# Kernel tuning notes

Measured on AMD Instinct MI355X. Metric: run time of the kernel, lower is better.

## Reference

```python
import jax, jax.numpy as jnp
import numpy as np

S = 2        # downscale
REDUCE = 32  # QK channel dim


def _to_grid(x):
    # [B,C,H,W] -> [B,C,H/S,W/S,S*S], matching ConverToGrid (reshape+permute+reshape)
    B, C, H, W = x.shape
    h, w = H // S, W // S
    x = x.reshape(B, C, h, S, w, S)
    x = x.transpose(0, 1, 2, 4, 3, 5)
    return x.reshape(B, C, h, w, S * S)


def setup_inputs() -> dict:
    key = jax.random.key(0)
    k1, k2, k3 = jax.random.split(key, 3)
    fm = jax.random.normal(k1, (8, 128, 256, 256), dtype=jnp.float32)
    Wq = jax.random.normal(k2, (REDUCE, 128), dtype=jnp.float32) * 0.05
    Wk = jax.random.normal(k3, (REDUCE, 128), dtype=jnp.float32) * 0.05
    return {"fm": fm, "Wq": Wq, "Wk": Wk}


def reference(fm, Wq, Wk):
    B, C, H, W = fm.shape
    h, w = H // S, W // S
    # Q branch: AvgPool2d(S,S) -> 1x1 conv -> scale by 1/sqrt(reduce)
    pooled = fm.reshape(B, C, h, S, w, S).mean(axis=(3, 5))          # [B,C,h,w]
    Q = jnp.einsum('rc,bchw->brhw', Wq, pooled) / jnp.sqrt(
        jnp.asarray(REDUCE, fm.dtype))                               # [B,r,h,w]
    # K branch: 1x1 conv -> grid
    K = _to_grid(jnp.einsum('rc,bchw->brhw', Wk, fm))                # [B,r,h,w,S*S]
    # V branch: grid of raw features
    V = _to_grid(fm)                                                 # [B,C,h,w,S*S]
    # sum over channel dim of Q*K, softmax over window dim (dropout p=0 => identity)
    logits = jnp.einsum('brhw,brhws->bhws', Q, K)                    # [B,h,w,S*S]
    attn = jax.nn.softmax(logits, axis=-1)
    # weighted sum over window positions
    out = jnp.einsum('bchws,bhws->bchw', V, attn)                    # [B,C,h,w]
    return out
```

## Files before the change

### kernel.cpp

```cpp
#include <hip/hip_runtime.h>
#include <hip/hip_bf16.h>
#include <math.h>


typedef unsigned int uint32;

__device__ __forceinline__ uint32 pack2(float x, float y) {
  union { __hip_bfloat162 h; uint32 u; } cvt;
  cvt.h = __float22bfloat162_rn(make_float2(x, y));
  return cvt.u;
}
__device__ __forceinline__ float2 unpack2(uint32 u) {
  float2 r;
  r.x = __uint_as_float(u << 16);
  r.y = __uint_as_float(u & 0xffff0000u);
  return r;
}

__global__ __launch_bounds__(256) void wt_kernel(const float* __restrict__ Wq,
                                                 const float* __restrict__ Wk,
                                                 float* __restrict__ ws) {
  int t = blockIdx.x * 256 + threadIdx.x;
  if (t < 4096) {
    int c = t >> 5, r = t & 31;
    ws[c * 32 + r]        = Wq[r * 128 + c] * (0.25f / sqrtf(32.0f));
    ws[4096 + c * 32 + r] = Wk[r * 128 + c];
  }
}

__global__ __launch_bounds__(512)
void attn_main(const float* __restrict__ fm,
               const float* __restrict__ ws,
               float* __restrict__ out) {
  __shared__ float Qpart[4 * 32 * 64];
  __shared__ float lbuf[8 * 64 * 4];
  __shared__ float abuf[64 * 4];

  const int tid = threadIdx.x;
  const int p   = tid & 63;
  const int g   = __builtin_amdgcn_readfirstlane(tid >> 6);

  const int blk = blockIdx.x;
  const int w0  = (blk & 1) * 64;
  const int h   = (blk >> 1) & 127;
  const int b   = blk >> 8;
  const int cb  = g * 16;

  const float* gbase = fm + ((size_t)(b * 128 + cb) * 65536) +
                       (size_t)(2 * h) * 256 + 2 * (w0 + p);
  const float* wq = ws + cb * 32;
  const float* wk = ws + 4096 + cb * 32;

  uint32 pka[16], pkb[16];
  {
    const float* gp = gbase;
#pragma unroll
    for (int i = 0; i < 16; ++i) {
      const float2 va = *(const float2*)(gp);
      const float2 vb = *(const float2*)(gp + 256);
      pka[i] = pack2(va.x, va.y);
      pkb[i] = pack2(vb.x, vb.y);
      gp += 65536;
    }
  }

  float qa[32];
#pragma unroll
  for (int r = 0; r < 32; ++r) qa[r] = 0.f;
#pragma unroll
  for (int i = 0; i < 16; ++i) {
    const float2 va = unpack2(pka[i]);
    const float2 vb = unpack2(pkb[i]);
    const float u = (va.x + va.y) + (vb.x + vb.y);
#pragma unroll
    for (int r = 0; r < 32; ++r)
      qa[r] = fmaf(wq[i * 32 + r], u, qa[r]);
  }

  if (g >= 4) {
#pragma unroll
    for (int r = 0; r < 32; ++r) Qpart[(g - 4) * 2048 + r * 64 + p] = qa[r];
  }
  __syncthreads();
  if (g < 4) {
#pragma unroll
    for (int r = 0; r < 32; ++r) Qpart[g * 2048 + r * 64 + p] += qa[r];
  }
  __syncthreads();
  if (g < 2) {
#pragma unroll
    for (int r = 0; r < 32; ++r)
      Qpart[g * 2048 + r * 64 + p] += Qpart[(g + 2) * 2048 + r * 64 + p];
  }
  __syncthreads();
#pragma unroll
  for (int r = 0; r < 32; ++r)
    qa[r] = Qpart[r * 64 + p] + Qpart[2048 + r * 64 + p];

  float l0 = 0.f, l1 = 0.f, l2 = 0.f, l3 = 0.f;
#pragma unroll
  for (int i = 0; i < 16; ++i) {
    const float2 va = unpack2(pka[i]);
    const float2 vb = unpack2(pkb[i]);
    float t0 = 0.f, t1 = 0.f;
#pragma unroll
    for (int r = 0; r < 32; r += 2) {
      t0 = fmaf(qa[r + 0], wk[i * 32 + r + 0], t0);
      t1 = fmaf(qa[r + 1], wk[i * 32 + r + 1], t1);
    }
    const float tv = t0 + t1;
    l0 = fmaf(tv, va.x, l0);
    l1 = fmaf(tv, va.y, l1);
    l2 = fmaf(tv, vb.x, l2);
    l3 = fmaf(tv, vb.y, l3);
  }
  *(float4*)(lbuf + (g * 64 + p) * 4) = make_float4(l0, l1, l2, l3);
  __syncthreads();

  if (tid < 64) {
    float L0 = 0.f, L1 = 0.f, L2 = 0.f, L3 = 0.f;
#pragma unroll
    for (int k = 0; k < 8; ++k) {
      const float4 s = *(const float4*)(lbuf + (k * 64 + tid) * 4);
      L0 += s.x; L1 += s.y; L2 += s.z; L3 += s.w;
    }
    const float mx = fmaxf(fmaxf(L0, L1), fmaxf(L2, L3));
    const float e0 = __expf(L0 - mx), e1 = __expf(L1 - mx);
    const float e2 = __expf(L2 - mx), e3 = __expf(L3 - mx);
    const float inv = 1.0f / ((e0 + e1) + (e2 + e3));
    *(float4*)(abuf + tid * 4) =
        make_float4(e0 * inv, e1 * inv, e2 * inv, e3 * inv);
  }
  __syncthreads();
  const float4 at = *(const float4*)(abuf + p * 4);

  {
    float* op = out + ((size_t)(b * 128 + cb) * 16384) + h * 128 + w0 + p;
#pragma unroll
    for (int i = 0; i < 16; ++i) {
      const float2 va = unpack2(pka[i]);
      const float2 vb = unpack2(pkb[i]);
      op[(size_t)i * 16384] =
          fmaf(at.x, va.x, fmaf(at.y, va.y, fmaf(at.z, vb.x, at.w * vb.y)));
    }
  }
}

extern "C" void kernel_launch(void* const* d_in, const int* in_sizes, int n_in,
                              void* d_out, int out_size, void* d_ws, size_t ws_size,
                              hipStream_t stream) {
  const float* fm = (const float*)d_in[0];
  const float* Wq = (const float*)d_in[1];
  const float* Wk = (const float*)d_in[2];
  float* outp = (float*)d_out;
  float* ws = (float*)d_ws;

  wt_kernel<<<16, 256, 0, stream>>>(Wq, Wk, ws);
  attn_main<<<2048, 512, 0, stream>>>(fm, ws, outp);
}
```

Measured before the change: 138.3 us.

## Stage packed fm tile and bf16 weights in LDS with 256-thread blocks

```diff
diff --git a/kernel.cpp b/kernel.cpp
--- a/kernel.cpp
+++ b/kernel.cpp
@@ -4,6 +4,8 @@
 
 
 typedef unsigned int uint32;
+typedef const __attribute__((address_space(1))) void* gas_t;
+typedef __attribute__((address_space(3))) void* las_t;
 
 __device__ __forceinline__ uint32 pack2(float x, float y) {
   union { __hip_bfloat162 h; uint32 u; } cvt;
@@ -19,111 +21,152 @@
 
 __global__ __launch_bounds__(256) void wt_kernel(const float* __restrict__ Wq,
                                                  const float* __restrict__ Wk,
-                                                 float* __restrict__ ws) {
+                                                 uint32* __restrict__ ws) {
   int t = blockIdx.x * 256 + threadIdx.x;
-  if (t < 4096) {
-    int c = t >> 5, r = t & 31;
-    ws[c * 32 + r]        = Wq[r * 128 + c] * (0.25f / sqrtf(32.0f));
-    ws[4096 + c * 32 + r] = Wk[r * 128 + c];
-  }
-}
-
-__global__ __launch_bounds__(512)
+  if (t < 2048) {
+    int c = t >> 4, j = t & 15;
+    const float s = 0.25f / sqrtf(32.0f);
+    ws[c * 16 + j] = pack2(Wq[(2 * j) * 128 + c] * s,
+                           Wq[(2 * j + 1) * 128 + c] * s);
+    ws[2048 + c * 16 + j] = pack2(Wk[(2 * j) * 128 + c],
+                                  Wk[(2 * j + 1) * 128 + c]);
+  }
+}
+
+__global__ __launch_bounds__(256, 4)
 void attn_main(const float* __restrict__ fm,
-               const float* __restrict__ ws,
+               const uint32* __restrict__ ws,
                float* __restrict__ out) {
-  __shared__ float Qpart[4 * 32 * 64];
-  __shared__ float lbuf[8 * 64 * 4];
-  __shared__ float abuf[64 * 4];
+  extern __shared__ char smem[];
+  uint2*  stash = (uint2*)smem;
+  uint32* wbuf  = (uint32*)(smem + 65536);
+  float*  Qbuf  = (float*)(smem + 73728);
+  float*  lbuf  = Qbuf;
+  float*  abuf  = Qbuf + 1024;
 
   const int tid = threadIdx.x;
   const int p   = tid & 63;
-  const int g   = __builtin_amdgcn_readfirstlane(tid >> 6);
+  const int w   = __builtin_amdgcn_readfirstlane(tid >> 6);
+  const int cb  = 32 * w;
 
   const int blk = blockIdx.x;
   const int w0  = (blk & 1) * 64;
   const int h   = (blk >> 1) & 127;
   const int b   = blk >> 8;
-  const int cb  = g * 16;
-
-  const float* gbase = fm + ((size_t)(b * 128 + cb) * 65536) +
-                       (size_t)(2 * h) * 256 + 2 * (w0 + p);
-  const float* wq = ws + cb * 32;
-  const float* wk = ws + 4096 + cb * 32;
-
-  uint32 pka[16], pkb[16];
-  {
-    const float* gp = gbase;
+
 #pragma unroll
-    for (int i = 0; i < 16; ++i) {
-      const float2 va = *(const float2*)(gp);
-      const float2 vb = *(const float2*)(gp + 256);
-      pka[i] = pack2(va.x, va.y);
-      pkb[i] = pack2(vb.x, vb.y);
-      gp += 65536;
+  for (int j = 0; j < 8; ++j) Qbuf[tid * 8 + j] = 0.f;
+
+  {
+    const char* src = (const char*)ws + tid * 16;
+    char* dst = (char*)wbuf + tid * 16;
+    __builtin_amdgcn_global_load_lds((gas_t)src, (las_t)dst, 16, 0, 0);
+    __builtin_amdgcn_global_load_lds((gas_t)(src + 4096), (las_t)(dst + 4096),
+                                     16, 0, 0);
+  }
+
+  {
+    const float* g = fm + ((size_t)(b * 128 + cb)) * 65536 +
+                     (size_t)(2 * h) * 256 + 2 * (w0 + p);
+#pragma unroll 8
+    for (int c = 0; c < 32; ++c) {
+      const float2 va = *(const float2*)(g + (size_t)c * 65536);
+      const float2 vb = *(const float2*)(g + (size_t)c * 65536 + 256);
+      stash[(cb + c) * 64 + p] =
+          make_uint2(pack2(va.x, va.y), pack2(vb.x, vb.y));
     }
   }
-
-  float qa[32];
+  asm volatile("s_waitcnt vmcnt(0)" ::: "memory");
+  __syncthreads();
+
+#define QFMA(word, r0)                              \
+  {                                                 \
+    const float2 f = unpack2(word);                 \
+    Qacc[r0] = fmaf(f.x, u, Qacc[r0]);              \
+    Qacc[(r0) + 1] = fmaf(f.y, u, Qacc[(r0) + 1]);  \
+  }
+
+  float Qacc[32];
 #pragma unroll
-  for (int r = 0; r < 32; ++r) qa[r] = 0.f;
+  for (int r = 0; r < 32; ++r) Qacc[r] = 0.f;
+#pragma unroll 4
+  for (int c = 0; c < 32; ++c) {
+    const int cc = cb + c;
+    const uint2 sv = stash[cc * 64 + p];
+    const float2 va = unpack2(sv.x);
+    const float2 vb = unpack2(sv.y);
+    const float u = (va.x + va.y) + (vb.x + vb.y);
+    const uint4 wa = *(const uint4*)(wbuf + cc * 16);
+    const uint4 wb = *(const uint4*)(wbuf + cc * 16 + 4);
+    const uint4 wc = *(const uint4*)(wbuf + cc * 16 + 8);
+    const uint4 wd = *(const uint4*)(wbuf + cc * 16 + 12);
+    QFMA(wa.x, 0)  QFMA(wa.y, 2)  QFMA(wa.z, 4)  QFMA(wa.w, 6)
+    QFMA(wb.x, 8)  QFMA(wb.y, 10) QFMA(wb.z, 12) QFMA(wb.w, 14)
+    QFMA(wc.x, 16) QFMA(wc.y, 18) QFMA(wc.z, 20) QFMA(wc.w, 22)
+    QFMA(wd.x, 24) QFMA(wd.y, 26) QFMA(wd.z, 28) QFMA(wd.w, 30)
+  }
+#undef QFMA
+  __syncthreads();
+
+  {
+    const char* src = (const char*)ws + 8192 + tid * 16;
+    char* dst = (char*)wbuf + tid * 16;
+    __builtin_amdgcn_global_load_lds((gas_t)src, (las_t)dst, 16, 0, 0);
+    __builtin_amdgcn_global_load_lds((gas_t)(src + 4096), (las_t)(dst + 4096),
+                                     16, 0, 0);
+  }
+#pragma unroll 8
+  for (int r = 0; r < 32; ++r) atomicAdd(&Qbuf[r * 64 + p], Qacc[r]);
+  asm volatile("s_waitcnt vmcnt(0)" ::: "memory");
+  __syncthreads();
+
+  float qh[32];
 #pragma unroll
-  for (int i = 0; i < 16; ++i) {
-    const float2 va = unpack2(pka[i]);
-    const float2 vb = unpack2(pkb[i]);
-    const float u = (va.x + va.y) + (vb.x + vb.y);
-#pragma unroll
-    for (int r = 0; r < 32; ++r)
-      qa[r] = fmaf(wq[i * 32 + r], u, qa[r]);
-  }
-
-  if (g >= 4) {
-#pragma unroll
-    for (int r = 0; r < 32; ++r) Qpart[(g - 4) * 2048 + r * 64 + p] = qa[r];
-  }
-  __syncthreads();
-  if (g < 4) {
-#pragma unroll
-    for (int r = 0; r < 32; ++r) Qpart[g * 2048 + r * 64 + p] += qa[r];
-  }
-  __syncthreads();
-  if (g < 2) {
-#pragma unroll
-    for (int r = 0; r < 32; ++r)
-      Qpart[g * 2048 + r * 64 + p] += Qpart[(g + 2) * 2048 + r * 64 + p];
-  }
-  __syncthreads();
-#pragma unroll
-  for (int r = 0; r < 32; ++r)
-    qa[r] = Qpart[r * 64 + p] + Qpart[2048 + r * 64 + p];
+  for (int r = 0; r < 32; ++r) qh[r] = Qbuf[r * 64 + p];
+  __syncthreads();
+
+#define TFMA(word, r0)                      \
+  {                                         \
+    const float2 f = unpack2(word);         \
+    t0 = fmaf(qh[r0], f.x, t0);             \
+    t1 = fmaf(qh[(r0) + 1], f.y, t1);       \
+  }
 
   float l0 = 0.f, l1 = 0.f, l2 = 0.f, l3 = 0.f;
-#pragma unroll
-  for (int i = 0; i < 16; ++i) {
-    const float2 va = unpack2(pka[i]);
-    const float2 vb = unpack2(pkb[i]);
+#pragma unroll 4
+  for (int c = 0; c < 32; ++c) {
+    const int cc = cb + c;
+    const uint4 wa = *(const uint4*)(wbuf + cc * 16);
+    const uint4 wb = *(const uint4*)(wbuf + cc * 16 + 4);
+    const uint4 wc = *(const uint4*)(wbuf + cc * 16 + 8);
+    const uint4 wd = *(const uint4*)(wbuf + cc * 16 + 12);
     float t0 = 0.f, t1 = 0.f;
-#pragma unroll
-    for (int r = 0; r < 32; r += 2) {
-      t0 = fmaf(qa[r + 0], wk[i * 32 + r + 0], t0);
-      t1 = fmaf(qa[r + 1], wk[i * 32 + r + 1], t1);
-    }
+    TFMA(wa.x, 0)  TFMA(wa.y, 2)  TFMA(wa.z, 4)  TFMA(wa.w, 6)
+    TFMA(wb.x, 8)  TFMA(wb.y, 10) TFMA(wb.z, 12) TFMA(wb.w, 14)
+    TFMA(wc.x, 16) TFMA(wc.y, 18) TFMA(wc.z, 20) TFMA(wc.w, 22)
+    TFMA(wd.x, 24) TFMA(wd.y, 26) TFMA(wd.z, 28) TFMA(wd.w, 30)
     const float tv = t0 + t1;
+    const uint2 sv = stash[cc * 64 + p];
+    const float2 va = unpack2(sv.x);
+    const float2 vb = unpack2(sv.y);
     l0 = fmaf(tv, va.x, l0);
     l1 = fmaf(tv, va.y, l1);
     l2 = fmaf(tv, vb.x, l2);
     l3 = fmaf(tv, vb.y, l3);
   }
-  *(float4*)(lbuf + (g * 64 + p) * 4) = make_float4(l0, l1, l2, l3);
+#undef TFMA
+  *(float4*)(lbuf + (w * 64 + p) * 4) = make_float4(l0, l1, l2, l3);
   __syncthreads();
 
   if (tid < 64) {
-    float L0 = 0.f, L1 = 0.f, L2 = 0.f, L3 = 0.f;
-#pragma unroll
-    for (int k = 0; k < 8; ++k) {
-      const float4 s = *(const float4*)(lbuf + (k * 64 + tid) * 4);
-      L0 += s.x; L1 += s.y; L2 += s.z; L3 += s.w;
-    }
+    const float4 s0 = *(const float4*)(lbuf + (0 * 64 + tid) * 4);
+    const float4 s1 = *(const float4*)(lbuf + (1 * 64 + tid) * 4);
+    const float4 s2 = *(const float4*)(lbuf + (2 * 64 + tid) * 4);
+    const float4 s3 = *(const float4*)(lbuf + (3 * 64 + tid) * 4);
+    const float L0 = (s0.x + s1.x) + (s2.x + s3.x);
+    const float L1 = (s0.y + s1.y) + (s2.y + s3.y);
+    const float L2 = (s0.z + s1.z) + (s2.z + s3.z);
+    const float L3 = (s0.w + s1.w) + (s2.w + s3.w);
     const float mx = fmaxf(fmaxf(L0, L1), fmaxf(L2, L3));
     const float e0 = __expf(L0 - mx), e1 = __expf(L1 - mx);
     const float e2 = __expf(L2 - mx), e3 = __expf(L3 - mx);
@@ -132,15 +175,16 @@
         make_float4(e0 * inv, e1 * inv, e2 * inv, e3 * inv);
   }
   __syncthreads();
-  const float4 at = *(const float4*)(abuf + p * 4);
-
-  {
-    float* op = out + ((size_t)(b * 128 + cb) * 16384) + h * 128 + w0 + p;
-#pragma unroll
-    for (int i = 0; i < 16; ++i) {
-      const float2 va = unpack2(pka[i]);
-      const float2 vb = unpack2(pkb[i]);
-      op[(size_t)i * 16384] =
+
+  {
+    const float4 at = *(const float4*)(abuf + p * 4);
+    float* op = out + ((size_t)(b * 128 + cb)) * 16384 + h * 128 + w0 + p;
+#pragma unroll 4
+    for (int c = 0; c < 32; ++c) {
+      const uint2 sv = stash[(cb + c) * 64 + p];
+      const float2 va = unpack2(sv.x);
+      const float2 vb = unpack2(sv.y);
+      op[(size_t)c * 16384] =
           fmaf(at.x, va.x, fmaf(at.y, va.y, fmaf(at.z, vb.x, at.w * vb.y)));
     }
   }
@@ -153,8 +197,13 @@
   const float* Wq = (const float*)d_in[1];
   const float* Wk = (const float*)d_in[2];
   float* outp = (float*)d_out;
-  float* ws = (float*)d_ws;
-
-  wt_kernel<<<16, 256, 0, stream>>>(Wq, Wk, ws);
-  attn_main<<<2048, 512, 0, stream>>>(fm, ws, outp);
-}
+  uint32* ws = (uint32*)d_ws;
+
+  const int smem_bytes = 81920;
+  (void)hipFuncSetAttribute((const void*)attn_main,
+                            hipFuncAttributeMaxDynamicSharedMemorySize,
+                            smem_bytes);
+
+  wt_kernel<<<8, 256, 0, stream>>>(Wq, Wk, ws);
+  attn_main<<<2048, 256, smem_bytes, stream>>>(fm, ws, outp);
+}
```

New measurement: 204.3 us. +47.7%, slower.
